# Kernel tuning notes

Measured on AMD Instinct MI355X. Metric: run time of the kernel, lower is better.

The kernel has to match this reference:

```python
import jax, jax.numpy as jnp
import numpy as np

N_NODES = 10000
N_EDGES = 160000
BATCH = 32
IN_FEAT = 64
POLY_K = 5
OUT_FEAT = 128


def setup_inputs() -> dict:
    key = jax.random.key(0)
    k_x, k_r, k_c, k_v, k_w, k_b = jax.random.split(key, 6)
    x = jax.random.normal(k_x, (BATCH, N_NODES, IN_FEAT), dtype=jnp.float32)
    lap_rows = jax.random.randint(k_r, (N_EDGES,), 0, N_NODES, dtype=jnp.int32)
    lap_cols = jax.random.randint(k_c, (N_EDGES,), 0, N_NODES, dtype=jnp.int32)
    # small values keep the degree-5 Chebyshev recurrence numerically tame
    lap_vals = jax.random.normal(k_v, (N_EDGES,), dtype=jnp.float32) * 0.05
    weight = jax.random.normal(k_w, (IN_FEAT * POLY_K, OUT_FEAT), dtype=jnp.float32) * 0.1
    bias = jax.random.normal(k_b, (1, 1, OUT_FEAT), dtype=jnp.float32) * 0.1
    return {"x": x, "lap_rows": lap_rows, "lap_cols": lap_cols,
            "lap_vals": lap_vals, "weight": weight, "bias": bias,
            "pooling_size": 4}


def _spmm(rows, cols, vals, m):
    # sparse [N,N] @ dense [N,M] via gather + segment_sum
    return jax.ops.segment_sum(vals[:, None] * m[cols], rows, num_segments=N_NODES)


def reference(x, lap_rows, lap_cols, lap_vals, weight, bias, pooling_size):
    B, N, F = x.shape
    K = POLY_K
    Fo = weight.shape[1]
    # x0: [N, F*B]
    x0 = jnp.transpose(x, (1, 2, 0)).reshape(N, F * B)
    terms = [x0]
    if K > 1:
        x1 = _spmm(lap_rows, lap_cols, lap_vals, x0)
        terms.append(x1)
        for _ in range(2, K):
            x2 = 2.0 * _spmm(lap_rows, lap_cols, lap_vals, x1) - x0
            terms.append(x2)
            x0, x1 = x1, x2
    xk = jnp.stack(terms, axis=0)                      # [K, N, F*B]
    xk = xk.reshape(K, N, F, B)
    xk = jnp.transpose(xk, (3, 1, 2, 0))               # [B, N, F, K]
    xk = xk.reshape(B * N, F * K)
    out = (xk @ weight).reshape(B, N, Fo)              # dense projection
    out = jax.nn.relu(out + bias)                      # bias + ReLU
    if pooling_size > 1:
        out = out.reshape(B, N // pooling_size, pooling_size, Fo).max(axis=2)
    return out
```

## Files before the change

kernel.cpp:

```cpp
#include <hip/hip_runtime.h>
#include <hip/hip_bf16.h>
#include <cstddef>
#include <cstdint>

#define N_NODES 10000
#define N_EDGES 160000
#define BATCH 32
#define IN_FEAT 64
#define POLY_K 5
#define OUT_FEAT 128
#define KTOT 320
#define POOLSZ 4
#define NPOOL 2500
#define KPAD 328

typedef short bf16x8 __attribute__((ext_vector_type(8)));
typedef unsigned short u16x8 __attribute__((ext_vector_type(8)));
typedef float f32x4 __attribute__((ext_vector_type(4)));

__device__ __forceinline__ unsigned short f2bf(float f) {
  unsigned int u = __float_as_uint(f);
  unsigned int r = u + 0x7FFFu + ((u >> 16) & 1u);
  return (unsigned short)(r >> 16);
}
__device__ __forceinline__ float bf2f(unsigned short u) {
  return __uint_as_float(((unsigned int)u) << 16);
}


__global__ void zero_int_kernel(int* __restrict__ p, int n) {
  int i = blockIdx.x * 256 + threadIdx.x;
  if (i < n) p[i] = 0;
}

__global__ void hist_kernel(const int* __restrict__ rows, int* __restrict__ deg) {
  int e = blockIdx.x * 256 + threadIdx.x;
  if (e < N_EDGES) atomicAdd(&deg[rows[e]], 1);
}

__global__ void scan_kernel(const int* __restrict__ deg, int* __restrict__ row_start,
                            int* __restrict__ cursor) {
  __shared__ int sm[1024];
  __shared__ int carry;
  int t = threadIdx.x;
  if (t == 0) { carry = 0; row_start[0] = 0; }
  __syncthreads();
  for (int base = 0; base < N_NODES; base += 1024) {
    int idx = base + t;
    int v = (idx < N_NODES) ? deg[idx] : 0;
    sm[t] = v;
    __syncthreads();
    for (int off = 1; off < 1024; off <<= 1) {
      int xv = 0;
      if (t >= off) xv = sm[t - off];
      __syncthreads();
      sm[t] += xv;
      __syncthreads();
    }
    if (idx < N_NODES) {
      int incl = sm[t];
      row_start[idx + 1] = carry + incl;
      cursor[idx] = carry + incl - v;
    }
    __syncthreads();
    if (t == 1023) carry += sm[1023];
    __syncthreads();
  }
}

__global__ void scatter_kernel(const int* __restrict__ rows, const int* __restrict__ cols,
                               const float* __restrict__ vals, int* __restrict__ cursor,
                               int* __restrict__ csr_cols, float* __restrict__ csr_vals) {
  int e = blockIdx.x * 256 + threadIdx.x;
  if (e < N_EDGES) {
    int r = rows[e];
    int p = atomicAdd(&cursor[r], 1);
    csr_cols[p] = cols[e];
    csr_vals[p] = vals[e];
  }
}


__global__ void wpack_kernel(const float* __restrict__ weight, unsigned short* __restrict__ wpack) {
  int id = blockIdx.x * 256 + threadIdx.x;
  if (id >= 5120) return;
  int ft = id / 640;
  int c = (id / 64) % 10;
  int l = id % 64;
  int fo = ft * 16 + (l & 15);
  unsigned short v[8];
  #pragma unroll
  for (int j = 0; j < 8; ++j) {
    int k = c * 32 + ((l >> 4)) * 8 + j;
    int row = (k & 63) * POLY_K + (k >> 6);
    v[j] = f2bf(weight[row * OUT_FEAT + fo]);
  }
  ushort4* dst = (ushort4*)&wpack[(size_t)id * 8];
  dst[0] = make_ushort4(v[0], v[1], v[2], v[3]);
  dst[1] = make_ushort4(v[4], v[5], v[6], v[7]);
}


template <int BB>
__global__ __launch_bounds__(256) void transpose_kernel(const float* __restrict__ x,
                                                        unsigned short* __restrict__ t0, int b0) {
  constexpr int CB = 64 * BB;
  int n = blockIdx.x;
  int t = threadIdx.x;
  for (int i = t * 8; i < CB; i += 2048) {
    int b = i >> 6;
    int f = i & 63;
    const float* xp = &x[((size_t)(b0 + b) * N_NODES + n) * IN_FEAT + f];
    float4 v0 = *(const float4*)xp;
    float4 v1 = *(const float4*)(xp + 4);
    u16x8 o;
    o[0] = f2bf(v0.x); o[1] = f2bf(v0.y); o[2] = f2bf(v0.z); o[3] = f2bf(v0.w);
    o[4] = f2bf(v1.x); o[5] = f2bf(v1.y); o[6] = f2bf(v1.z); o[7] = f2bf(v1.w);
    *(u16x8*)&t0[(size_t)n * CB + i] = o;
  }
}


template <int BB>
__global__ __launch_bounds__(256) void spmm_kernel(const unsigned short* __restrict__ xin,
                                                   const unsigned short* __restrict__ prev,
                                                   unsigned short* __restrict__ xout,
                                                   const int* __restrict__ row_start,
                                                   const int* __restrict__ csr_cols,
                                                   const float* __restrict__ csr_vals,
                                                   float alpha, int use_prev) {
  constexpr int CB = 64 * BB;
  constexpr int SCOLS = CB / 8;
  constexpr int LPR = SCOLS / 8;
  constexpr int RPB = 256 / LPR;
  int bid = blockIdx.x;
  int slice = bid & 7;
  int rowblk = bid >> 3;
  int t = threadIdx.x;
  int rl = t / LPR;
  int cl = t % LPR;
  int n = rowblk * RPB + rl;
  if (n >= N_NODES) return;
  int off = slice * SCOLS + cl * 8;

  int s = row_start[n];
  int e = row_start[n + 1];
  float acc[8];
  #pragma unroll
  for (int j = 0; j < 8; ++j) acc[j] = 0.f;

  int i = s;
  for (; i + 3 < e; i += 4) {
    int c0 = csr_cols[i + 0], c1 = csr_cols[i + 1];
    int c2 = csr_cols[i + 2], c3 = csr_cols[i + 3];
    float v0 = csr_vals[i + 0], v1 = csr_vals[i + 1];
    float v2 = csr_vals[i + 2], v3 = csr_vals[i + 3];
    u16x8 p0 = *(const u16x8*)&xin[(size_t)c0 * CB + off];
    u16x8 p1 = *(const u16x8*)&xin[(size_t)c1 * CB + off];
    u16x8 p2 = *(const u16x8*)&xin[(size_t)c2 * CB + off];
    u16x8 p3 = *(const u16x8*)&xin[(size_t)c3 * CB + off];
    #pragma unroll
    for (int j = 0; j < 8; ++j) {
      acc[j] = fmaf(v0, bf2f(p0[j]), acc[j]);
      acc[j] = fmaf(v1, bf2f(p1[j]), acc[j]);
      acc[j] = fmaf(v2, bf2f(p2[j]), acc[j]);
      acc[j] = fmaf(v3, bf2f(p3[j]), acc[j]);
    }
  }
  for (; i < e; ++i) {
    int c0 = csr_cols[i];
    float v0 = csr_vals[i];
    u16x8 p0 = *(const u16x8*)&xin[(size_t)c0 * CB + off];
    #pragma unroll
    for (int j = 0; j < 8; ++j) acc[j] = fmaf(v0, bf2f(p0[j]), acc[j]);
  }

  u16x8 o;
  if (use_prev) {
    u16x8 q = *(const u16x8*)&prev[(size_t)n * CB + off];
    #pragma unroll
    for (int j = 0; j < 8; ++j) o[j] = f2bf(alpha * acc[j] - bf2f(q[j]));
  } else {
    #pragma unroll
    for (int j = 0; j < 8; ++j) o[j] = f2bf(alpha * acc[j]);
  }
  *(u16x8*)&xout[(size_t)n * CB + off] = o;
}


template <int BB>
__global__ __launch_bounds__(256) void gemm_mfma_kernel(const unsigned short* __restrict__ slices,
                                                        const unsigned short* __restrict__ wpack,
                                                        const float* __restrict__ bias,
                                                        float* __restrict__ out, int b0) {
  constexpr int CB = 64 * BB;
  constexpr int MB = (BB >= 16) ? 16 : BB;
  constexpr int MT = MB / 4;
  constexpr int SPAN = MB * 64;
  constexpr size_t SLICE = (size_t)N_NODES * CB;
  __shared__ unsigned short A[4 * MB * KPAD];

  int g = blockIdx.x;
  int bh = blockIdx.y;
  int t = threadIdx.x;

  constexpr int SLOTS = POLY_K * 4 * (SPAN / 8);
  for (int idx = t; idx < SLOTS; idx += 256) {
    int kpoly = idx / (4 * (SPAN / 8));
    int r = idx % (4 * (SPAN / 8));
    int nd = r / (SPAN / 8);
    int colloc = (r % (SPAN / 8)) * 8;
    int bloc = colloc >> 6;
    int f = colloc & 63;
    u16x8 v = *(const u16x8*)&slices[(size_t)kpoly * SLICE +
                                     (size_t)(g * POOLSZ + nd) * CB + bh * SPAN + colloc];
    *(u16x8*)&A[(bloc * 4 + nd) * KPAD + kpoly * 64 + f] = v;
  }
  __syncthreads();

  int w = t >> 6;
  int l = t & 63;
  int lm = l & 15;
  int q = l >> 4;

  f32x4 acc[MT][2];
  #pragma unroll
  for (int mt = 0; mt < MT; ++mt)
    #pragma unroll
    for (int fj = 0; fj < 2; ++fj) {
      acc[mt][fj][0] = 0.f; acc[mt][fj][1] = 0.f;
      acc[mt][fj][2] = 0.f; acc[mt][fj][3] = 0.f;
    }

  #pragma unroll
  for (int c = 0; c < 10; ++c) {
    bf16x8 bfrag[2];
    #pragma unroll
    for (int fj = 0; fj < 2; ++fj) {
      int fi = w * 2 + fj;
      bfrag[fj] = *(const bf16x8*)&wpack[(size_t)(((fi * 10) + c) * 64 + l) * 8];
    }
    #pragma unroll
    for (int mt = 0; mt < MT; ++mt) {
      bf16x8 afrag = *(const bf16x8*)&A[(mt * 16 + lm) * KPAD + c * 32 + q * 8];
      acc[mt][0] = __builtin_amdgcn_mfma_f32_16x16x32_bf16(afrag, bfrag[0], acc[mt][0], 0, 0, 0);
      acc[mt][1] = __builtin_amdgcn_mfma_f32_16x16x32_bf16(afrag, bfrag[1], acc[mt][1], 0, 0, 0);
    }
  }

  #pragma unroll
  for (int fj = 0; fj < 2; ++fj) {
    int fo = (w * 2 + fj) * 16 + lm;
    float bv = bias[fo];
    #pragma unroll
    for (int mt = 0; mt < MT; ++mt) {
      float mx = fmaxf(fmaxf(acc[mt][fj][0], acc[mt][fj][1]),
                       fmaxf(acc[mt][fj][2], acc[mt][fj][3]));
      float val = fmaxf(mx + bv, 0.f);
      int b = b0 + bh * MB + mt * 4 + q;
      out[((size_t)b * NPOOL + g) * OUT_FEAT + fo] = val;
    }
  }
}


template <int BB>
static void run_pipeline(const float* x, const float* bias,
                         const int* row_start, const int* csr_cols, const float* csr_vals,
                         const unsigned short* wpack,
                         unsigned short* slices, float* out, hipStream_t stream) {
  constexpr int CB = 64 * BB;
  constexpr size_t SLICE = (size_t)N_NODES * CB;
  constexpr int LPR = (CB / 8) / 8;
  constexpr int RPB = 256 / LPR;
  constexpr int NBLK = ((N_NODES + RPB - 1) / RPB) * 8;
  constexpr int MB = (BB >= 16) ? 16 : BB;
  for (int b0 = 0; b0 < BATCH; b0 += BB) {
    transpose_kernel<BB><<<N_NODES, 256, 0, stream>>>(x, slices, b0);
    for (int k = 1; k < POLY_K; ++k) {
      const unsigned short* xin  = slices + (size_t)(k - 1) * SLICE;
      const unsigned short* prev = (k >= 2) ? slices + (size_t)(k - 2) * SLICE : slices;
      unsigned short* xout = slices + (size_t)k * SLICE;
      float alpha = (k == 1) ? 1.0f : 2.0f;
      spmm_kernel<BB><<<NBLK, 256, 0, stream>>>(xin, prev, xout, row_start,
                                                csr_cols, csr_vals, alpha,
                                                (k >= 2) ? 1 : 0);
    }
    gemm_mfma_kernel<BB><<<dim3(NPOOL, BB / MB), 256, 0, stream>>>(slices, wpack, bias, out, b0);
  }
}

static size_t needed_bytes(int BB) {
  return 1482112u + (size_t)6400000 * BB;
}

extern "C" void kernel_launch(void* const* d_in, const int* in_sizes, int n_in,
                              void* d_out, int out_size, void* d_ws, size_t ws_size,
                              hipStream_t stream) {
  const float* x        = (const float*)d_in[0];
  const int*   lap_rows = (const int*)d_in[1];
  const int*   lap_cols = (const int*)d_in[2];
  const float* lap_vals = (const float*)d_in[3];
  const float* weight   = (const float*)d_in[4];
  const float* bias     = (const float*)d_in[5];
  float* out = (float*)d_out;

  int* deg       = (int*)d_ws;
  int* cursor    = deg + 10016;
  int* row_start = cursor + 10016;
  int* csr_cols  = row_start + 10016;
  float* csr_vals = (float*)(csr_cols + N_EDGES);
  unsigned short* wpack = (unsigned short*)(csr_vals + N_EDGES);
  unsigned short* slices = wpack + 40960;

  int BB = 0;
  if      (ws_size >= needed_bytes(32)) BB = 32;
  else if (ws_size >= needed_bytes(16)) BB = 16;
  else if (ws_size >= needed_bytes(8))  BB = 8;
  else if (ws_size >= needed_bytes(4))  BB = 4;
  if (BB == 0) return;

  zero_int_kernel<<<(N_NODES + 255) / 256, 256, 0, stream>>>(deg, N_NODES);
  hist_kernel<<<(N_EDGES + 255) / 256, 256, 0, stream>>>(lap_rows, deg);
  scan_kernel<<<1, 1024, 0, stream>>>(deg, row_start, cursor);
  scatter_kernel<<<(N_EDGES + 255) / 256, 256, 0, stream>>>(lap_rows, lap_cols, lap_vals,
                                                            cursor, csr_cols, csr_vals);
  wpack_kernel<<<20, 256, 0, stream>>>(weight, wpack);

  switch (BB) {
    case 32: run_pipeline<32>(x, bias, row_start, csr_cols, csr_vals, wpack, slices, out, stream); break;
    case 16: run_pipeline<16>(x, bias, row_start, csr_cols, csr_vals, wpack, slices, out, stream); break;
    case 8:  run_pipeline<8>(x, bias, row_start, csr_cols, csr_vals, wpack, slices, out, stream); break;
    case 4:  run_pipeline<4>(x, bias, row_start, csr_cols, csr_vals, wpack, slices, out, stream); break;
  }
}
```

Measured before the change: 463.4 us.

## Use direct global-to-LDS loads with XOR swizzle in GEMM; split SpMM into 16 slices

The GEMM staging loop now uses global_load_lds to copy slice data straight into an unpadded LDS tile. An XOR swizzle on the 16-byte chunk index replaces padding to avoid bank conflicts on MFMA fragment reads, and launch bounds request 4 waves per SIMD. The SpMM kernel splits columns into 16 slices instead of 8, mapped in phases so consecutive blocks hit different XCDs, which should improve L2 locality of the gathered rows. The global_load_lds addressing assumes each wave writes a contiguous 1 KB LDS region, so it depends on the chunk count being a multiple of 256.

```diff
diff --git a/kernel.cpp b/kernel.cpp
--- a/kernel.cpp
+++ b/kernel.cpp
@@ -12,7 +12,6 @@
 #define KTOT 320
 #define POOLSZ 4
 #define NPOOL 2500
-#define KPAD 328
 
 typedef short bf16x8 __attribute__((ext_vector_type(8)));
 typedef unsigned short u16x8 __attribute__((ext_vector_type(8)));
@@ -130,15 +129,21 @@
                                                    const float* __restrict__ csr_vals,
                                                    float alpha, int use_prev) {
   constexpr int CB = 64 * BB;
-  constexpr int SCOLS = CB / 8;
+  constexpr int NS = 16;
+  constexpr int SCOLS = CB / NS;
   constexpr int LPR = SCOLS / 8;
   constexpr int RPB = 256 / LPR;
+  constexpr int RB = (N_NODES + RPB - 1) / RPB;
+  constexpr int PHB = RB * 8;
   int bid = blockIdx.x;
-  int slice = bid & 7;
-  int rowblk = bid >> 3;
+  int phase = bid / PHB;
+  int rem = bid - phase * PHB;
+  int xcd = rem & 7;
+  int rowblk = rem >> 3;
+  int slice = phase * 8 + xcd;
   int t = threadIdx.x;
   int rl = t / LPR;
-  int cl = t % LPR;
+  int cl = t - rl * LPR;
   int n = rowblk * RPB + rl;
   if (n >= N_NODES) return;
   int off = slice * SCOLS + cl * 8;
@@ -189,32 +194,38 @@
 
 
 template <int BB>
-__global__ __launch_bounds__(256) void gemm_mfma_kernel(const unsigned short* __restrict__ slices,
-                                                        const unsigned short* __restrict__ wpack,
-                                                        const float* __restrict__ bias,
-                                                        float* __restrict__ out, int b0) {
+__global__ __launch_bounds__(256, 4) void gemm_mfma_kernel(const unsigned short* __restrict__ slices,
+                                                           const unsigned short* __restrict__ wpack,
+                                                           const float* __restrict__ bias,
+                                                           float* __restrict__ out, int b0) {
   constexpr int CB = 64 * BB;
   constexpr int MB = (BB >= 16) ? 16 : BB;
   constexpr int MT = MB / 4;
   constexpr int SPAN = MB * 64;
+  constexpr int ROWS = 4 * MB;
   constexpr size_t SLICE = (size_t)N_NODES * CB;
-  __shared__ unsigned short A[4 * MB * KPAD];
+  __shared__ unsigned short A[ROWS * 320];
 
   int g = blockIdx.x;
   int bh = blockIdx.y;
   int t = threadIdx.x;
 
-  constexpr int SLOTS = POLY_K * 4 * (SPAN / 8);
-  for (int idx = t; idx < SLOTS; idx += 256) {
-    int kpoly = idx / (4 * (SPAN / 8));
-    int r = idx % (4 * (SPAN / 8));
-    int nd = r / (SPAN / 8);
-    int colloc = (r % (SPAN / 8)) * 8;
-    int bloc = colloc >> 6;
-    int f = colloc & 63;
-    u16x8 v = *(const u16x8*)&slices[(size_t)kpoly * SLICE +
-                                     (size_t)(g * POOLSZ + nd) * CB + bh * SPAN + colloc];
-    *(u16x8*)&A[(bloc * 4 + nd) * KPAD + kpoly * 64 + f] = v;
+  constexpr int CHUNKS = ROWS * 40;
+  for (int idx0 = 0; idx0 < CHUNKS; idx0 += 256) {
+    int idx = idx0 + t;
+    int row = idx / 40;
+    int cphys = idx - row * 40;
+    int clog = cphys ^ (row & 7);
+    int kpoly = clog >> 3;
+    int fb = (clog & 7) * 8;
+    int bloc = row >> 2;
+    int nd = row & 3;
+    const unsigned short* gsrc = &slices[(size_t)kpoly * SLICE +
+                                         (size_t)(g * POOLSZ + nd) * CB + bh * SPAN + bloc * 64 + fb];
+    unsigned short* lbase = &A[(size_t)(idx0 + (t & 192)) * 8];
+    __builtin_amdgcn_global_load_lds((const __attribute__((address_space(1))) unsigned int*)gsrc,
+                                     (__attribute__((address_space(3))) unsigned int*)lbase,
+                                     16, 0, 0);
   }
   __syncthreads();
 
@@ -222,6 +233,7 @@
   int l = t & 63;
   int lm = l & 15;
   int q = l >> 4;
+  int swz = lm & 7;
 
   f32x4 acc[MT][2];
   #pragma unroll
@@ -242,7 +254,7 @@
     }
     #pragma unroll
     for (int mt = 0; mt < MT; ++mt) {
-      bf16x8 afrag = *(const bf16x8*)&A[(mt * 16 + lm) * KPAD + c * 32 + q * 8];
+      bf16x8 afrag = *(const bf16x8*)&A[(mt * 16 + lm) * 320 + (((c * 4 + q) ^ swz) << 3)];
       acc[mt][0] = __builtin_amdgcn_mfma_f32_16x16x32_bf16(afrag, bfrag[0], acc[mt][0], 0, 0, 0);
       acc[mt][1] = __builtin_amdgcn_mfma_f32_16x16x32_bf16(afrag, bfrag[1], acc[mt][1], 0, 0, 0);
     }
@@ -271,9 +283,9 @@
                          unsigned short* slices, float* out, hipStream_t stream) {
   constexpr int CB = 64 * BB;
   constexpr size_t SLICE = (size_t)N_NODES * CB;
-  constexpr int LPR = (CB / 8) / 8;
+  constexpr int LPR = (CB / 16) / 8;
   constexpr int RPB = 256 / LPR;
-  constexpr int NBLK = ((N_NODES + RPB - 1) / RPB) * 8;
+  constexpr int NBLK = ((N_NODES + RPB - 1) / RPB) * 16;
   constexpr int MB = (BB >= 16) ? 16 : BB;
   for (int b0 = 0; b0 < BATCH; b0 += BB) {
     transpose_kernel<BB><<<N_NODES, 256, 0, stream>>>(x, slices, b0);
```

After: 464.2 us. About the same (+0.2%).
